# Kernel optimization log

Measured on AMD Instinct MI355X. Metric: run time of the kernel, lower is better.

Reference implementation:

```python
import jax, jax.numpy as jnp
import numpy as np

B, D, E, H1, H2 = 64, 2048, 64, 512, 256
EPS = 1e-5


def setup_inputs() -> dict:
    key = jax.random.key(0)
    ks = jax.random.split(key, 8)
    s = lambda k, shape, scale: jax.random.normal(k, shape, dtype=jnp.float32) * scale
    return {
        "sparse_representation": s(ks[0], (B, D), 1.0),
        "emb": s(ks[1], (D, E), 1.0),
        "W1": s(ks[2], (D + E, H1), (D + E) ** -0.5),
        "b1": s(ks[3], (H1,), 0.02),
        "g1": jnp.ones((H1,), jnp.float32),
        "beta1": jnp.zeros((H1,), jnp.float32),
        "m1": jnp.zeros((H1,), jnp.float32),
        "v1": jnp.ones((H1,), jnp.float32),
        "W2": s(ks[4], (H1, H2), H1 ** -0.5),
        "b2": s(ks[5], (H2,), 0.02),
        "g2": jnp.ones((H2,), jnp.float32),
        "beta2": jnp.zeros((H2,), jnp.float32),
        "m2": jnp.zeros((H2,), jnp.float32),
        "v2": jnp.ones((H2,), jnp.float32),
        "W3": s(ks[6], (H2, 1), H2 ** -0.5),
        "b3": s(ks[7], (1,), 0.02),
    }


def _bn_relu(x, g, beta, m, v):
    # eval-mode BatchNorm1d followed by ReLU
    return jax.nn.relu((x - m) * jax.lax.rsqrt(v + EPS) * g + beta)


def reference(sparse_representation, emb, W1, b1, g1, beta1, m1, v1,
              W2, b2, g2, beta2, m2, v2, W3, b3):
    rep = sparse_representation  # (B, D)
    W1d, W1e = W1[:D], W1[D:]    # (D, H1), (E, H1)
    # Fused predict_all: for each k, masked input zeros column k, so
    # Linear(masked_k) = rep @ W1d - rep[:, k] * W1d[k]
    base = rep @ W1d + b1                       # (B, H1)
    emb_h = emb @ W1e                           # (D, H1) per-index embedding contribution
    h1 = base[:, None, :] + emb_h[None, :, :] - rep[:, :, None] * W1d[None, :, :]  # (B, D, H1)
    h1 = _bn_relu(h1, g1, beta1, m1, v1)
    h2 = jnp.einsum("bkh,ho->bko", h1, W2) + b2  # (B, D, H2)
    h2 = _bn_relu(h2, g2, beta2, m2, v2)
    out = jnp.einsum("bkh,h->bk", h2, W3[:, 0]) + b3[0]  # (B, D)
    return out
```

## Files before the change

kernel.cpp:

```cpp
#include <hip/hip_runtime.h>
#include <hip/hip_bf16.h>

#define EPS 1e-5f

typedef __attribute__((ext_vector_type(8))) short short8;
typedef __attribute__((ext_vector_type(4))) float f32x4;

__device__ __forceinline__ float bflo(unsigned u) { return __uint_as_float(u << 16); }
__device__ __forceinline__ float bfhi(unsigned u) { return __uint_as_float(u & 0xffff0000u); }
__device__ __forceinline__ unsigned short f2bf(float f) {
  unsigned u = __float_as_uint(f);
  u = u + 0x7FFFu + ((u >> 16) & 1u);
  return (unsigned short)(u >> 16);
}
__device__ __forceinline__ unsigned pack2(float a, float b) {
  return (unsigned)f2bf(a) | ((unsigned)f2bf(b) << 16);
}
__device__ __forceinline__ unsigned pk2(float lo, float hi) {
  __hip_bfloat162 h = __float22bfloat162_rn(float2{lo, hi});
  union { __hip_bfloat162 h2; unsigned u; } cv;
  cv.h2 = h;
  return cv.u;
}

__global__ __launch_bounds__(256) void prep2(
    const float* __restrict__ emb, const float* __restrict__ W1,
    const float* __restrict__ g1, const float* __restrict__ v1,
    const float* __restrict__ b1, const float* __restrict__ m1,
    const float* __restrict__ beta1,
    const float* __restrict__ W2,
    const float* __restrict__ g2, const float* __restrict__ v2,
    const float* __restrict__ b2, const float* __restrict__ m2,
    const float* __restrict__ beta2,
    unsigned* __restrict__ Q, unsigned* __restrict__ R,
    unsigned short* __restrict__ W2t,
    float* __restrict__ t2, float* __restrict__ c2, float* __restrict__ Pf) {
  __shared__ float smem[256];
  const int x = blockIdx.x, t = threadIdx.x;
  if (x < 512) {
    const int k0 = x * 4;
    smem[t] = emb[x * 256 + t];
    __syncthreads();
    const int h = t * 2;
    const float a0 = g1[h] * rsqrtf(v1[h] + EPS);
    const float a1 = g1[h + 1] * rsqrtf(v1[h + 1] + EPS);
    const float pb0 = a0 * (b1[h] - m1[h]) + beta1[h];
    const float pb1 = a1 * (b1[h + 1] - m1[h + 1]) + beta1[h + 1];
    const float* We = W1 + 2048 * 512;
    float acc0[4], acc1[4];
    #pragma unroll
    for (int k = 0; k < 4; ++k) { acc0[k] = 0.f; acc1[k] = 0.f; }
    #pragma unroll 4
    for (int e = 0; e < 64; ++e) {
      float2 wv = *(const float2*)(We + e * 512 + h);
      #pragma unroll
      for (int k = 0; k < 4; ++k) {
        float ev = smem[k * 64 + e];
        acc0[k] = fmaf(ev, wv.x, acc0[k]);
        acc1[k] = fmaf(ev, wv.y, acc1[k]);
      }
    }
    #pragma unroll
    for (int k = 0; k < 4; ++k) {
      Q[(k0 + k) * 256 + t] = pack2(a0 * acc0[k] + pb0, a1 * acc1[k] + pb1);
      float2 wv = *(const float2*)(W1 + (size_t)(k0 + k) * 512 + h);
      R[(k0 + k) * 256 + t] = pack2(a0 * wv.x, a1 * wv.y);
    }
  } else if (x < 576) {
    const int h0 = (x - 512) * 8;
    const int o = t;
    unsigned d[4];
    #pragma unroll
    for (int i = 0; i < 4; ++i) {
      float v0 = W2[(h0 + 2 * i) * 256 + o];
      float v1_ = W2[(h0 + 2 * i + 1) * 256 + o];
      d[i] = pack2(v0, v1_);
    }
    *(uint4*)(W2t + o * 512 + h0) = make_uint4(d[0], d[1], d[2], d[3]);
  } else {
    float tv = g2[t] * rsqrtf(v2[t] + EPS);
    t2[t] = tv;
    c2[t] = tv * (b2[t] - m2[t]) + beta2[t];
    f32x4 z = (f32x4){0.f, 0.f, 0.f, 0.f};
    #pragma unroll 8
    for (int j = 0; j < 32; ++j)
      *(f32x4*)(Pf + ((size_t)(j * 256 + t)) * 4) = z;
  }
}

__global__ __launch_bounds__(256) void p_gemm(
    const float* __restrict__ rep, const unsigned* __restrict__ R,
    float* __restrict__ Pf) {
  __shared__ float red[4][512];
  const int b = blockIdx.x >> 3, ksl = blockIdx.x & 7;
  const int t = threadIdx.x, lane = t & 63, kq = t >> 6;
  const int kbase = ksl * 256 + kq * 64;
  const unsigned* Rp = R + (size_t)kbase * 256 + lane * 4;
  const float* rp = rep + b * 2048 + kbase;
  float acc[8];
  #pragma unroll
  for (int i = 0; i < 8; ++i) acc[i] = 0.f;
  #pragma unroll 8
  for (int k = 0; k < 64; ++k) {
    uint4 rv = *(const uint4*)(Rp + (size_t)k * 256);
    float rk = rp[k];
    acc[0] = fmaf(rk, bflo(rv.x), acc[0]); acc[1] = fmaf(rk, bfhi(rv.x), acc[1]);
    acc[2] = fmaf(rk, bflo(rv.y), acc[2]); acc[3] = fmaf(rk, bfhi(rv.y), acc[3]);
    acc[4] = fmaf(rk, bflo(rv.z), acc[4]); acc[5] = fmaf(rk, bfhi(rv.z), acc[5]);
    acc[6] = fmaf(rk, bflo(rv.w), acc[6]); acc[7] = fmaf(rk, bfhi(rv.w), acc[7]);
  }
  *(f32x4*)(&red[kq][lane * 8])     = (f32x4){acc[0], acc[1], acc[2], acc[3]};
  *(f32x4*)(&red[kq][lane * 8 + 4]) = (f32x4){acc[4], acc[5], acc[6], acc[7]};
  __syncthreads();
  {
    const int h = t * 2;
    float s0 = red[0][h] + red[1][h] + red[2][h] + red[3][h];
    float s1 = red[0][h + 1] + red[1][h + 1] + red[2][h + 1] + red[3][h + 1];
    atomicAdd(&Pf[b * 512 + h], s0);
    atomicAdd(&Pf[b * 512 + h + 1], s1);
  }
}

__global__ __launch_bounds__(256) void pf2p(const float* __restrict__ Pf,
                                            unsigned* __restrict__ P) {
  const int i = blockIdx.x * 256 + threadIdx.x;
  float2 v = *(const float2*)(Pf + 2 * i);
  P[i] = pack2(v.x, v.y);
}

__global__ __launch_bounds__(256, 2) void fused_main(
    const float* __restrict__ rep,
    const unsigned* __restrict__ P,
    const unsigned* __restrict__ Q,
    const unsigned* __restrict__ Rm,
    const unsigned short* __restrict__ W2t,
    const float* __restrict__ t2, const float* __restrict__ c2,
    const float* __restrict__ W3, const float* __restrict__ b3,
    float* __restrict__ out) {
  __shared__ unsigned short A_lds[2][8192];
  __shared__ float partial[4][128];

  const int t = threadIdx.x;
  const int w = t >> 6;
  const int ln = t & 15;
  const int lq = (t >> 4) & 3;
  const int ks_id = w & 1;
  const int hi_id = w >> 1;
  const int k0 = blockIdx.x * 2;

  float rb[4];
  #pragma unroll
  for (int p = 0; p < 4; ++p) {
    int r = (p * 2 + hi_id) * 16 + ln;
    rb[p] = rep[(r & 63) * 2048 + k0 + (r >> 6)];
  }

  f32x4 acc[8][4];
  #pragma unroll
  for (int mi = 0; mi < 8; ++mi)
    #pragma unroll
    for (int nj = 0; nj < 4; ++nj) acc[mi][nj] = (f32x4){0.f, 0.f, 0.f, 0.f};

  uint4 s_p[4], s_q[4], s_r[4];
  short8 bfr0[4], bfr1[4];

  auto genLoad = [&](int c) {
    const int cb2 = (c * 64 + ks_id * 32 + lq * 8) >> 1;
    #pragma unroll
    for (int p = 0; p < 4; ++p) {
      const int r = (p * 2 + hi_id) * 16 + ln;
      const int bb = r & 63;
      const int kg = k0 + (r >> 6);
      s_p[p] = *(const uint4*)(P + (bb << 8) + cb2);
      s_q[p] = *(const uint4*)(Q + (kg << 8) + cb2);
      s_r[p] = *(const uint4*)(Rm + (kg << 8) + cb2);
    }
  };
  auto genStore = [&](unsigned short* buf) {
    #pragma unroll
    for (int p = 0; p < 4; ++p) {
      const float rp_ = rb[p];
      unsigned d[4];
      float z0, z1;
      z0 = fmaf(-rp_, bflo(s_r[p].x), bflo(s_p[p].x) + bflo(s_q[p].x));
      z1 = fmaf(-rp_, bfhi(s_r[p].x), bfhi(s_p[p].x) + bfhi(s_q[p].x));
      d[0] = pk2(fmaxf(z0, 0.f), fmaxf(z1, 0.f));
      z0 = fmaf(-rp_, bflo(s_r[p].y), bflo(s_p[p].y) + bflo(s_q[p].y));
      z1 = fmaf(-rp_, bfhi(s_r[p].y), bfhi(s_p[p].y) + bfhi(s_q[p].y));
      d[1] = pk2(fmaxf(z0, 0.f), fmaxf(z1, 0.f));
      z0 = fmaf(-rp_, bflo(s_r[p].z), bflo(s_p[p].z) + bflo(s_q[p].z));
      z1 = fmaf(-rp_, bfhi(s_r[p].z), bfhi(s_p[p].z) + bfhi(s_q[p].z));
      d[2] = pk2(fmaxf(z0, 0.f), fmaxf(z1, 0.f));
      z0 = fmaf(-rp_, bflo(s_r[p].w), bflo(s_p[p].w) + bflo(s_q[p].w));
      z1 = fmaf(-rp_, bfhi(s_r[p].w), bfhi(s_p[p].w) + bfhi(s_q[p].w));
      d[3] = pk2(fmaxf(z0, 0.f), fmaxf(z1, 0.f));
      *(uint4*)(&buf[(size_t)(p * 256 + t) * 8]) = make_uint4(d[0], d[1], d[2], d[3]);
    }
  };
  auto loadB = [&](int c, int ks, short8 (&bfr)[4]) {
    #pragma unroll
    for (int nj = 0; nj < 4; ++nj)
      bfr[nj] = *(const short8*)(W2t + (size_t)(w * 64 + nj * 16 + ln) * 512 +
                                 c * 64 + ks * 32 + lq * 8);
  };
  auto mfma_half = [&](const unsigned short* buf, int ks, short8 (&bfr)[4]) {
    short8 afr[4];
    #pragma unroll
    for (int mi = 0; mi < 4; ++mi)
      afr[mi] = *(const short8*)(buf + (size_t)((((mi * 2 + ks) * 4 + lq) * 16 + ln) * 8));
    #pragma unroll
    for (int mi = 0; mi < 4; ++mi)
      #pragma unroll
      for (int nj = 0; nj < 4; ++nj)
        acc[mi][nj] = __builtin_amdgcn_mfma_f32_16x16x32_bf16(afr[mi], bfr[nj], acc[mi][nj], 0, 0, 0);
    #pragma unroll
    for (int mi = 0; mi < 4; ++mi)
      afr[mi] = *(const short8*)(buf + (size_t)(((((mi + 4) * 2 + ks) * 4 + lq) * 16 + ln) * 8));
    #pragma unroll
    for (int mi = 0; mi < 4; ++mi)
      #pragma unroll
      for (int nj = 0; nj < 4; ++nj)
        acc[mi + 4][nj] = __builtin_amdgcn_mfma_f32_16x16x32_bf16(afr[mi], bfr[nj], acc[mi + 4][nj], 0, 0, 0);
  };

  genLoad(0);
  genStore(A_lds[0]);
  genLoad(1);
  loadB(0, 0, bfr0);
  loadB(0, 1, bfr1);

  for (int c = 0; c < 8; ++c) {
    __syncthreads();
    if (c < 7) genStore(A_lds[(c + 1) & 1]);
    if (c < 6) genLoad(c + 2);
    const unsigned short* buf = A_lds[c & 1];
    mfma_half(buf, 0, bfr0);
    if (c < 7) loadB(c + 1, 0, bfr0);
    mfma_half(buf, 1, bfr1);
    if (c < 7) loadB(c + 1, 1, bfr1);
  }

  float t2v[4], c2v[4], w3v[4];
  #pragma unroll
  for (int nj = 0; nj < 4; ++nj) {
    int o = w * 64 + nj * 16 + ln;
    t2v[nj] = t2[o];
    c2v[nj] = c2[o];
    w3v[nj] = W3[o];
  }
  #pragma unroll
  for (int mi = 0; mi < 8; ++mi) {
    float s[4] = {0.f, 0.f, 0.f, 0.f};
    #pragma unroll
    for (int nj = 0; nj < 4; ++nj)
      #pragma unroll
      for (int r = 0; r < 4; ++r) {
        float u = fmaf(t2v[nj], acc[mi][nj][r], c2v[nj]);
        u = fmaxf(u, 0.f);
        s[r] = fmaf(u, w3v[nj], s[r]);
      }
    #pragma unroll
    for (int r = 0; r < 4; ++r) {
      #pragma unroll
      for (int m = 1; m < 16; m <<= 1) s[r] += __shfl_xor(s[r], m, 64);
    }
    if (ln == 0) {
      #pragma unroll
      for (int r = 0; r < 4; ++r) partial[w][mi * 16 + lq * 4 + r] = s[r];
    }
  }
  __syncthreads();
  if (t < 128) {
    out[(t & 63) * 2048 + k0 + (t >> 6)] =
        partial[0][t] + partial[1][t] + partial[2][t] + partial[3][t] + b3[0];
  }
}

extern "C" void kernel_launch(void* const* d_in, const int* in_sizes, int n_in,
                              void* d_out, int out_size, void* d_ws, size_t ws_size,
                              hipStream_t stream) {
  const float* rep   = (const float*)d_in[0];
  const float* emb   = (const float*)d_in[1];
  const float* W1    = (const float*)d_in[2];
  const float* b1    = (const float*)d_in[3];
  const float* g1    = (const float*)d_in[4];
  const float* beta1 = (const float*)d_in[5];
  const float* m1    = (const float*)d_in[6];
  const float* v1    = (const float*)d_in[7];
  const float* W2    = (const float*)d_in[8];
  const float* b2    = (const float*)d_in[9];
  const float* g2    = (const float*)d_in[10];
  const float* beta2 = (const float*)d_in[11];
  const float* m2    = (const float*)d_in[12];
  const float* v2    = (const float*)d_in[13];
  const float* W3    = (const float*)d_in[14];
  const float* b3    = (const float*)d_in[15];
  float* out = (float*)d_out;
  char* ws = (char*)d_ws;

  float* Pf            = (float*)(ws + 0);
  unsigned* P          = (unsigned*)(ws + 131072);
  unsigned* Q          = (unsigned*)(ws + 196608);
  unsigned* R          = (unsigned*)(ws + 2293760);
  unsigned short* W2t  = (unsigned short*)(ws + 4390912);
  float* t2            = (float*)(ws + 4653056);
  float* c2            = (float*)(ws + 4654080);

  prep2<<<577, 256, 0, stream>>>(emb, W1, g1, v1, b1, m1, beta1, W2, g2, v2,
                                 b2, m2, beta2, Q, R, W2t, t2, c2, Pf);
  p_gemm<<<512, 256, 0, stream>>>(rep, R, Pf);
  pf2p<<<64, 256, 0, stream>>>(Pf, P);
  fused_main<<<1024, 256, 0, stream>>>(rep, P, Q, R, W2t, t2, c2, W3, b3, out);
}
```

Baseline: 161.3 us.

## Merge prep, P-GEMM and P conversion into one launch with last-block reduction

Folds the weight-prep kernel, the rep@W1 partial GEMM and the fp32-to-bf16 conversion into a single kernel. The GEMM blocks now read fp32 W1 directly instead of waiting on the bf16 R buffer. Each block writes its split-K partial to a scratch slice, and the last block per batch row, found through an atomic counter, sums the partials, applies the BN scale and packs P. This drops two kernel launches and the float atomics, at the cost of a memset, twice the W1 read bandwidth in the GEMM part, and a threadfence-based cross-block handoff.

```diff
diff --git a/kernel.cpp b/kernel.cpp
--- a/kernel.cpp
+++ b/kernel.cpp
@@ -23,8 +23,9 @@
   return cv.u;
 }
 
-__global__ __launch_bounds__(256) void prep2(
-    const float* __restrict__ emb, const float* __restrict__ W1,
+__global__ __launch_bounds__(256) void mega_prep(
+    const float* __restrict__ rep, const float* __restrict__ emb,
+    const float* __restrict__ W1,
     const float* __restrict__ g1, const float* __restrict__ v1,
     const float* __restrict__ b1, const float* __restrict__ m1,
     const float* __restrict__ beta1,
@@ -34,12 +35,15 @@
     const float* __restrict__ beta2,
     unsigned* __restrict__ Q, unsigned* __restrict__ R,
     unsigned short* __restrict__ W2t,
-    float* __restrict__ t2, float* __restrict__ c2, float* __restrict__ Pf) {
-  __shared__ float smem[256];
+    float* __restrict__ t2, float* __restrict__ c2,
+    float* __restrict__ Pf8, unsigned* __restrict__ P,
+    int* __restrict__ cnt) {
+  __shared__ float sbuf[2048];
+  __shared__ int done_s;
   const int x = blockIdx.x, t = threadIdx.x;
   if (x < 512) {
     const int k0 = x * 4;
-    smem[t] = emb[x * 256 + t];
+    sbuf[t] = emb[x * 256 + t];
     __syncthreads();
     const int h = t * 2;
     const float a0 = g1[h] * rsqrtf(v1[h] + EPS);
@@ -55,7 +59,7 @@
       float2 wv = *(const float2*)(We + e * 512 + h);
       #pragma unroll
       for (int k = 0; k < 4; ++k) {
-        float ev = smem[k * 64 + e];
+        float ev = sbuf[k * 64 + e];
         acc0[k] = fmaf(ev, wv.x, acc0[k]);
         acc1[k] = fmaf(ev, wv.y, acc1[k]);
       }
@@ -77,55 +81,54 @@
       d[i] = pack2(v0, v1_);
     }
     *(uint4*)(W2t + o * 512 + h0) = make_uint4(d[0], d[1], d[2], d[3]);
-  } else {
+  } else if (x == 576) {
     float tv = g2[t] * rsqrtf(v2[t] + EPS);
     t2[t] = tv;
     c2[t] = tv * (b2[t] - m2[t]) + beta2[t];
-    f32x4 z = (f32x4){0.f, 0.f, 0.f, 0.f};
+  } else {
+    const int i = x - 577, b = i >> 3, ksl = i & 7;
+    const int lane = t & 63, kq = t >> 6;
+    const int kbase = ksl * 256 + kq * 64;
+    const float* Wp = W1 + (size_t)kbase * 512 + lane * 8;
+    const float* rp = rep + b * 2048 + kbase;
+    float acc[8];
+    #pragma unroll
+    for (int j = 0; j < 8; ++j) acc[j] = 0.f;
     #pragma unroll 8
-    for (int j = 0; j < 32; ++j)
-      *(f32x4*)(Pf + ((size_t)(j * 256 + t)) * 4) = z;
-  }
-}
-
-__global__ __launch_bounds__(256) void p_gemm(
-    const float* __restrict__ rep, const unsigned* __restrict__ R,
-    float* __restrict__ Pf) {
-  __shared__ float red[4][512];
-  const int b = blockIdx.x >> 3, ksl = blockIdx.x & 7;
-  const int t = threadIdx.x, lane = t & 63, kq = t >> 6;
-  const int kbase = ksl * 256 + kq * 64;
-  const unsigned* Rp = R + (size_t)kbase * 256 + lane * 4;
-  const float* rp = rep + b * 2048 + kbase;
-  float acc[8];
-  #pragma unroll
-  for (int i = 0; i < 8; ++i) acc[i] = 0.f;
-  #pragma unroll 8
-  for (int k = 0; k < 64; ++k) {
-    uint4 rv = *(const uint4*)(Rp + (size_t)k * 256);
-    float rk = rp[k];
-    acc[0] = fmaf(rk, bflo(rv.x), acc[0]); acc[1] = fmaf(rk, bfhi(rv.x), acc[1]);
-    acc[2] = fmaf(rk, bflo(rv.y), acc[2]); acc[3] = fmaf(rk, bfhi(rv.y), acc[3]);
-    acc[4] = fmaf(rk, bflo(rv.z), acc[4]); acc[5] = fmaf(rk, bfhi(rv.z), acc[5]);
-    acc[6] = fmaf(rk, bflo(rv.w), acc[6]); acc[7] = fmaf(rk, bfhi(rv.w), acc[7]);
-  }
-  *(f32x4*)(&red[kq][lane * 8])     = (f32x4){acc[0], acc[1], acc[2], acc[3]};
-  *(f32x4*)(&red[kq][lane * 8 + 4]) = (f32x4){acc[4], acc[5], acc[6], acc[7]};
-  __syncthreads();
-  {
+    for (int k = 0; k < 64; ++k) {
+      float4 w0 = *(const float4*)(Wp + (size_t)k * 512);
+      float4 w1v = *(const float4*)(Wp + (size_t)k * 512 + 4);
+      float rk = rp[k];
+      acc[0] = fmaf(rk, w0.x, acc[0]);  acc[1] = fmaf(rk, w0.y, acc[1]);
+      acc[2] = fmaf(rk, w0.z, acc[2]);  acc[3] = fmaf(rk, w0.w, acc[3]);
+      acc[4] = fmaf(rk, w1v.x, acc[4]); acc[5] = fmaf(rk, w1v.y, acc[5]);
+      acc[6] = fmaf(rk, w1v.z, acc[6]); acc[7] = fmaf(rk, w1v.w, acc[7]);
+    }
+    float(*red)[512] = (float(*)[512])sbuf;
+    *(f32x4*)(&red[kq][lane * 8])     = (f32x4){acc[0], acc[1], acc[2], acc[3]};
+    *(f32x4*)(&red[kq][lane * 8 + 4]) = (f32x4){acc[4], acc[5], acc[6], acc[7]};
+    __syncthreads();
     const int h = t * 2;
     float s0 = red[0][h] + red[1][h] + red[2][h] + red[3][h];
     float s1 = red[0][h + 1] + red[1][h + 1] + red[2][h + 1] + red[3][h + 1];
-    atomicAdd(&Pf[b * 512 + h], s0);
-    atomicAdd(&Pf[b * 512 + h + 1], s1);
-  }
-}
-
-__global__ __launch_bounds__(256) void pf2p(const float* __restrict__ Pf,
-                                            unsigned* __restrict__ P) {
-  const int i = blockIdx.x * 256 + threadIdx.x;
-  float2 v = *(const float2*)(Pf + 2 * i);
-  P[i] = pack2(v.x, v.y);
+    *(float2*)(Pf8 + (size_t)(ksl * 64 + b) * 512 + h) = make_float2(s0, s1);
+    __threadfence();
+    __syncthreads();
+    if (t == 0) done_s = atomicAdd(&cnt[b], 1);
+    __syncthreads();
+    if (done_s == 7) {
+      __threadfence();
+      float p0 = 0.f, p1 = 0.f;
+      #pragma unroll
+      for (int s = 0; s < 8; ++s) {
+        float2 v = *(const float2*)(Pf8 + (size_t)(s * 64 + b) * 512 + h);
+        p0 += v.x; p1 += v.y;
+      }
+      const float a0 = g1[h] * rsqrtf(v1[h] + EPS);
+      const float a1 = g1[h + 1] * rsqrtf(v1[h + 1] + EPS);
+      P[b * 256 + t] = pack2(a0 * p0, a1 * p1);
+    }
+  }
 }
 
 __global__ __launch_bounds__(256, 2) void fused_main(
@@ -298,17 +301,18 @@
   float* out = (float*)d_out;
   char* ws = (char*)d_ws;
 
-  float* Pf            = (float*)(ws + 0);
-  unsigned* P          = (unsigned*)(ws + 131072);
-  unsigned* Q          = (unsigned*)(ws + 196608);
-  unsigned* R          = (unsigned*)(ws + 2293760);
-  unsigned short* W2t  = (unsigned short*)(ws + 4390912);
-  float* t2            = (float*)(ws + 4653056);
-  float* c2            = (float*)(ws + 4654080);
-
-  prep2<<<577, 256, 0, stream>>>(emb, W1, g1, v1, b1, m1, beta1, W2, g2, v2,
-                                 b2, m2, beta2, Q, R, W2t, t2, c2, Pf);
-  p_gemm<<<512, 256, 0, stream>>>(rep, R, Pf);
-  pf2p<<<64, 256, 0, stream>>>(Pf, P);
+  float* Pf8           = (float*)(ws + 0);
+  unsigned* P          = (unsigned*)(ws + 1048576);
+  unsigned* Q          = (unsigned*)(ws + 1114112);
+  unsigned* R          = (unsigned*)(ws + 3211264);
+  unsigned short* W2t  = (unsigned short*)(ws + 5308416);
+  float* t2            = (float*)(ws + 5570560);
+  float* c2            = (float*)(ws + 5571584);
+  int* cnt             = (int*)(ws + 5572608);
+
+  hipMemsetAsync(cnt, 0, 256, stream);
+  mega_prep<<<1089, 256, 0, stream>>>(rep, emb, W1, g1, v1, b1, m1, beta1, W2,
+                                      g2, v2, b2, m2, beta2, Q, R, W2t, t2, c2,
+                                      Pf8, P, cnt);
   fused_main<<<1024, 256, 0, stream>>>(rep, P, Q, R, W2t, t2, c2, W3, b3, out);
 }
```

New measurement: 213.6 us. +32.5%, slower.
